# Performance work log

Hardware: AMD Instinct MI355X
Metric: run time of the kernel (lower is better)

## Reference

```python
import jax, jax.numpy as jnp
import numpy as np

B, C, N, K = 8, 192, 3136, 9
COUT = 384


def setup_inputs() -> dict:
    key = jax.random.key(0)
    k1, k2, k3, k4 = jax.random.split(key, 4)
    x = jax.random.normal(k1, (B, C, N, 1), dtype=jnp.float32)
    edge_index = jax.random.randint(k2, (2, B, N, K), 0, N, dtype=jnp.int64)
    # 1x1 conv params: BasicConv([2C, COUT]) with bias, act='relu'
    W = jax.random.normal(k3, (COUT, 2 * C), dtype=jnp.float32) * (1.0 / np.sqrt(2 * C))
    b = jax.random.normal(k4, (COUT,), dtype=jnp.float32) * 0.01
    return {"x": x, "edge_index": edge_index, "W": W, "b": b}


def _gather(xs, idx):
    # xs: [B, C, N]; idx: [B, N, K] -> [B, C, N, K]
    return jax.vmap(lambda xb, ib: xb[:, ib])(xs, idx)


def reference(x, edge_index, W, b):
    xs = x[..., 0]                       # [B, C, N]
    x_i = _gather(xs, edge_index[1])     # [B, C, N, K] center features
    x_j = _gather(xs, edge_index[0])     # [B, C, N, K] neighbor features
    feat = jnp.concatenate([x_i, x_j - x_i], axis=1)  # [B, 2C, N, K]
    # 1x1 conv + bias + relu
    h = jnp.einsum('oi,bink->bonk', W, feat) + b[None, :, None, None]
    h = jax.nn.relu(h)                   # [B, COUT, N, K]
    return jnp.max(h, axis=-1, keepdims=True)  # [B, COUT, N, 1]
```

## Files before the change

### kernel.cpp

```cpp
#include <hip/hip_runtime.h>
#include <hip/hip_bf16.h>


#define Bb   8
#define Cc   192
#define Nn   3136
#define Kk   9
#define CO   384
#define TWOC 384
#define JTOT 768
#define PADC 200

typedef short  short8 __attribute__((ext_vector_type(8)));
typedef float  f32x4  __attribute__((ext_vector_type(4)));

__device__ __forceinline__ float bf2f(unsigned int u16) {
    union { unsigned int i; float f; } c;
    c.i = u16 << 16;
    return c.f;
}
__device__ __forceinline__ float bflo(unsigned int u) {
    union { unsigned int i; float f; } c;
    c.i = u << 16;
    return c.f;
}
__device__ __forceinline__ float bfhi(unsigned int u) {
    union { unsigned int i; float f; } c;
    c.i = u & 0xffff0000u;
    return c.f;
}
__device__ __forceinline__ short f2bf(float f) {
    __hip_bfloat16 h = __float2bfloat16(f);
    short s; __builtin_memcpy(&s, &h, 2); return s;
}
__device__ __forceinline__ void gload16(const void* g, void* l) {
    __builtin_amdgcn_global_load_lds(
        (const __attribute__((address_space(1))) unsigned int*)g,
        (__attribute__((address_space(3))) unsigned int*)l, 16, 0, 0);
}

__global__ __launch_bounds__(256) void prep_fused(const void* __restrict__ x_,
                                                  const void* __restrict__ W_,
                                                  const int* __restrict__ ei,
                                                  short* __restrict__ xT,
                                                  short* __restrict__ A_Tb,
                                                  int* __restrict__ flags) {
    __shared__ float s[64][33];
    __shared__ int sflag;
    const int tid = threadIdx.x;
    const int bid = blockIdx.x;

    if (tid < 64) {
        unsigned int u = ((const unsigned short*)x_)[2 * tid];
        int bige = (((u >> 7) & 0xFFu) >= 0x88u);
        unsigned long long bf = __ballot(bige);
        int f32 = (bf != 0ull) ? 1 : 0;
        if (tid == 0) sflag = f32;
        if (bid == 0) {
            int oddnz = (ei[2 * tid + 1] != 0);
            unsigned long long bo = __ballot(oddnz);
            if (tid == 0) {
                flags[0] = f32;
                flags[1] = (bo == 0ull) ? 1 : 0;
            }
        }
    }
    __syncthreads();
    const int fp32 = sflag;

    if (bid < 2352) {
        int b   = bid / 294;
        int rem = bid - b * 294;
        int ct  = rem / 49;
        int nt  = rem - ct * 49;
        const int n0 = nt * 64;
        const int c0 = ct * 32;
        const int cl   = tid >> 3;
        const int nseg = tid & 7;

        if (fp32) {
            const float* p = (const float*)x_ + ((size_t)b * Cc + c0 + cl) * Nn + n0 + nseg * 8;
            float4 v0 = *(const float4*)p;
            float4 v1 = *(const float4*)(p + 4);
            int nb = nseg * 8;
            s[nb + 0][cl] = v0.x;  s[nb + 1][cl] = v0.y;
            s[nb + 2][cl] = v0.z;  s[nb + 3][cl] = v0.w;
            s[nb + 4][cl] = v1.x;  s[nb + 5][cl] = v1.y;
            s[nb + 6][cl] = v1.z;  s[nb + 7][cl] = v1.w;
        } else {
            const unsigned short* p = (const unsigned short*)x_ + ((size_t)b * Cc + c0 + cl) * Nn + n0 + nseg * 8;
            ushort4 u0 = *(const ushort4*)p;
            ushort4 u1 = *(const ushort4*)(p + 4);
            int nb = nseg * 8;
            s[nb + 0][cl] = bf2f(u0.x);  s[nb + 1][cl] = bf2f(u0.y);
            s[nb + 2][cl] = bf2f(u0.z);  s[nb + 3][cl] = bf2f(u0.w);
            s[nb + 4][cl] = bf2f(u1.x);  s[nb + 5][cl] = bf2f(u1.y);
            s[nb + 6][cl] = bf2f(u1.z);  s[nb + 7][cl] = bf2f(u1.w);
        }
        __syncthreads();

        const int nl = tid >> 2;
        const int cs = tid & 3;
        short8 o;
#pragma unroll
        for (int i = 0; i < 8; ++i) o[i] = f2bf(s[nl][cs * 8 + i]);
        *(short8*)(xT + ((size_t)b * Nn + n0 + nl) * PADC + c0 + cs * 8) = o;
    } else {
        int t = (bid - 2352) * 256 + tid;
        int j = t / Cc;
        int c = t - j * Cc;
        int row = (j < CO) ? j : (j - CO);
        float w1, w2;
        if (fp32) {
            const float* W = (const float*)W_;
            w1 = W[row * TWOC + c];  w2 = W[row * TWOC + Cc + c];
        } else {
            const unsigned short* W = (const unsigned short*)W_;
            w1 = bf2f(W[row * TWOC + c]);  w2 = bf2f(W[row * TWOC + Cc + c]);
        }
        A_Tb[(size_t)j * PADC + c] = f2bf((j < CO) ? (w1 - w2) : w2);
    }
}

__global__ __launch_bounds__(256, 3) void gemm_mfma(const short* __restrict__ xT,
                                                    const short* __restrict__ A_Tb,
                                                    short* __restrict__ T) {
    __shared__ short Asl[64 * PADC];
    __shared__ short Bsl[64 * PADC];

    const int n0 = blockIdx.x * 64;
    const int j0 = blockIdx.y * 64;
    const int b  = blockIdx.z;
    const int tid  = threadIdx.x;
    const int w    = tid >> 6;
    const int lane = tid & 63;
    const int col  = lane & 15;
    const int quad = lane >> 4;

    {
        const short* gA = xT   + ((size_t)b * Nn + n0) * PADC;
        const short* gB = A_Tb + (size_t)j0 * PADC;
#pragma unroll
        for (int c = w; c < 25; c += 4) {
            gload16(gA + c * 512 + lane * 8, Asl + c * 512);
            gload16(gB + c * 512 + lane * 8, Bsl + c * 512);
        }
    }
    __syncthreads();

    f32x4 acc[4];
#pragma unroll
    for (int i = 0; i < 4; ++i) acc[i] = (f32x4)(0.0f);

#pragma unroll
    for (int kf = 0; kf < 6; ++kf) {
        short8 bfr = *(const short8*)(Bsl + (w * 16 + col) * PADC + kf * 32 + quad * 8);
#pragma unroll
        for (int fm = 0; fm < 4; ++fm) {
            short8 a = *(const short8*)(Asl + (fm * 16 + col) * PADC + kf * 32 + quad * 8);
            acc[fm] = __builtin_amdgcn_mfma_f32_16x16x32_bf16(a, bfr, acc[fm], 0, 0, 0);
        }
    }
    __syncthreads();

    short* Ct = Asl;
#pragma unroll
    for (int fm = 0; fm < 4; ++fm) {
#pragma unroll
        for (int r = 0; r < 4; ++r) {
            Ct[(fm * 16 + quad * 4 + r) * 72 + w * 16 + col] = f2bf(acc[fm][r]);
        }
    }
    __syncthreads();

    {
        const int row = tid >> 2;
        const int gq  = tid & 3;
#pragma unroll
        for (int i = 0; i < 2; ++i) {
            int g = gq + i * 4;
            *(short8*)(T + ((size_t)(b * Nn + n0 + row)) * JTOT + j0 + g * 8) =
                *(const short8*)(Ct + row * 72 + g * 8);
        }
    }
}

__global__ __launch_bounds__(384) void gather_max(const int* __restrict__ ei,
                                                  const short* __restrict__ T,
                                                  const void* __restrict__ bias_,
                                                  void* __restrict__ out_,
                                                  const int* __restrict__ flags) {
    __shared__ float sm[32][97];
    __shared__ int soff0[32][Kk];
    __shared__ int soff1[32][Kk];

    const int fp32 = flags[0];
    const int is64 = flags[1];
    const int bid  = blockIdx.x;
    const int b    = bid & 7;
    const int rest = bid >> 3;
    const int quarter = rest / 98;
    const int n0   = (rest % 98) * 32;
    const int tid  = threadIdx.x;

    for (int s = tid; s < 32 * 2 * Kk; s += 384) {
        int ln = s / (2 * Kk);
        int slot = s - ln * (2 * Kk);
        int n = n0 + ln;
        size_t pos; int* dstp;
        if (slot < Kk) { pos = ((size_t)b * Nn + n) * Kk + slot;               dstp = &soff0[ln][slot]; }
        else           { pos = ((size_t)(Bb + b) * Nn + n) * Kk + (slot - Kk); dstp = &soff1[ln][slot - Kk]; }
        int v = is64 ? ei[2 * pos] : ei[pos];
        v = (v < 0) ? 0 : (v >= Nn ? Nn - 1 : v);
        *dstp = v * (JTOT * 2);
    }
    __syncthreads();

    const int cg  = tid % 12;
    const int seg = tid / 12;
    const int och = quarter * 96 + cg * 8;
    const char* Tb = (const char*)T + (size_t)b * Nn * JTOT * 2;
    const char* Tu = Tb + (size_t)och * 2;
    const char* Tv = Tb + (size_t)(CO + och) * 2;

    float bv[8];
    if (fp32) {
        const float* bp = (const float*)bias_ + och;
#pragma unroll
        for (int j = 0; j < 8; ++j) bv[j] = bp[j];
    } else {
        const unsigned short* bp = (const unsigned short*)bias_ + och;
#pragma unroll
        for (int j = 0; j < 8; ++j) bv[j] = bf2f(bp[j]);
    }

    float m0 = -INFINITY, m1 = -INFINITY, m2 = -INFINITY, m3 = -INFINITY;
    float m4 = -INFINITY, m5 = -INFINITY, m6 = -INFINITY, m7 = -INFINITY;
#pragma unroll
    for (int k = 0; k < Kk; ++k) {
        const int o1 = soff1[seg][k];
        const int o0 = soff0[seg][k];
        uint4 uu = *(const uint4*)(Tu + o1);
        uint4 vv = *(const uint4*)(Tv + o0);
        m0 = fmaxf(m0, bflo(uu.x) + bflo(vv.x));
        m1 = fmaxf(m1, bfhi(uu.x) + bfhi(vv.x));
        m2 = fmaxf(m2, bflo(uu.y) + bflo(vv.y));
        m3 = fmaxf(m3, bfhi(uu.y) + bfhi(vv.y));
        m4 = fmaxf(m4, bflo(uu.z) + bflo(vv.z));
        m5 = fmaxf(m5, bfhi(uu.z) + bfhi(vv.z));
        m6 = fmaxf(m6, bflo(uu.w) + bflo(vv.w));
        m7 = fmaxf(m7, bfhi(uu.w) + bfhi(vv.w));
    }
    sm[seg][cg * 8 + 0] = fmaxf(m0 + bv[0], 0.0f);
    sm[seg][cg * 8 + 1] = fmaxf(m1 + bv[1], 0.0f);
    sm[seg][cg * 8 + 2] = fmaxf(m2 + bv[2], 0.0f);
    sm[seg][cg * 8 + 3] = fmaxf(m3 + bv[3], 0.0f);
    sm[seg][cg * 8 + 4] = fmaxf(m4 + bv[4], 0.0f);
    sm[seg][cg * 8 + 5] = fmaxf(m5 + bv[5], 0.0f);
    sm[seg][cg * 8 + 6] = fmaxf(m6 + bv[6], 0.0f);
    sm[seg][cg * 8 + 7] = fmaxf(m7 + bv[7], 0.0f);
    __syncthreads();

    const int g = tid >> 5, l = tid & 31;
    if (fp32) {
        float* op = (float*)out_;
#pragma unroll
        for (int rr = 0; rr < 8; ++rr) {
            int ol = g * 8 + rr;
            int o  = quarter * 96 + ol;
            op[((size_t)b * CO + o) * Nn + n0 + l] = sm[l][ol];
        }
    } else {
        __hip_bfloat16* op = (__hip_bfloat16*)out_;
#pragma unroll
        for (int rr = 0; rr < 8; ++rr) {
            int ol = g * 8 + rr;
            int o  = quarter * 96 + ol;
            op[((size_t)b * CO + o) * Nn + n0 + l] = __float2bfloat16(sm[l][ol]);
        }
    }
}

extern "C" void kernel_launch(void* const* d_in, const int* in_sizes, int n_in,
                              void* d_out, int out_size, void* d_ws, size_t ws_size,
                              hipStream_t stream) {
    const void* x  = d_in[0];
    const int*  ei = (const int*)d_in[1];
    const void* W  = d_in[2];
    const void* bs = d_in[3];

    char* ws = (char*)d_ws;
    int*   flags = (int*)ws;
    short* A_Tb  = (short*)(ws + 1024);
    short* xT    = (short*)(ws + (512u << 10));
    short* T     = (short*)(ws + (11u << 20));

    prep_fused<<<2352 + 576, 256, 0, stream>>>(x, W, ei, xT, A_Tb, flags);

    dim3 g1(Nn / 64, JTOT / 64, Bb);
    gemm_mfma<<<g1, 256, 0, stream>>>(xT, A_Tb, T);

    gather_max<<<Bb * 4 * (Nn / 32), 384, 0, stream>>>(ei, T, bs, d_out, flags);
}
```

Measured before the change: 132.4 us.

## Fuse prep, GEMM and gather-max into one persistent cooperative kernel

```diff
diff --git a/kernel.cpp b/kernel.cpp
--- a/kernel.cpp
+++ b/kernel.cpp
@@ -1,5 +1,8 @@
 #include <hip/hip_runtime.h>
 #include <hip/hip_bf16.h>
+#include <hip/hip_cooperative_groups.h>
+
+namespace cg = cooperative_groups;
 
 
 #define Bb   8
@@ -39,244 +42,253 @@
         (__attribute__((address_space(3))) unsigned int*)l, 16, 0, 0);
 }
 
-__global__ __launch_bounds__(256) void prep_fused(const void* __restrict__ x_,
-                                                  const void* __restrict__ W_,
-                                                  const int* __restrict__ ei,
-                                                  short* __restrict__ xT,
-                                                  short* __restrict__ A_Tb,
-                                                  int* __restrict__ flags) {
-    __shared__ float s[64][33];
-    __shared__ int sflag;
+__global__ __launch_bounds__(256, 3) void fused_all(
+    const void* __restrict__ x_, const int* __restrict__ ei,
+    const void* __restrict__ W_, const void* __restrict__ bias_,
+    void* __restrict__ out_, short* __restrict__ xT,
+    short* __restrict__ A_Tb, short* __restrict__ T)
+{
+    cg::grid_group grid = cg::this_grid();
+    __shared__ char smem[51200];
+    __shared__ int sflag, sis64;
     const int tid = threadIdx.x;
     const int bid = blockIdx.x;
+    const int nblk = gridDim.x;
 
     if (tid < 64) {
         unsigned int u = ((const unsigned short*)x_)[2 * tid];
         int bige = (((u >> 7) & 0xFFu) >= 0x88u);
         unsigned long long bf = __ballot(bige);
-        int f32 = (bf != 0ull) ? 1 : 0;
-        if (tid == 0) sflag = f32;
-        if (bid == 0) {
-            int oddnz = (ei[2 * tid + 1] != 0);
-            unsigned long long bo = __ballot(oddnz);
-            if (tid == 0) {
-                flags[0] = f32;
-                flags[1] = (bo == 0ull) ? 1 : 0;
-            }
-        }
+        if (tid == 0) sflag = (bf != 0ull) ? 1 : 0;
+        int oddnz = (ei[2 * tid + 1] != 0);
+        unsigned long long bo = __ballot(oddnz);
+        if (tid == 0) sis64 = (bo == 0ull) ? 1 : 0;
     }
     __syncthreads();
     const int fp32 = sflag;
-
-    if (bid < 2352) {
-        int b   = bid / 294;
-        int rem = bid - b * 294;
-        int ct  = rem / 49;
-        int nt  = rem - ct * 49;
-        const int n0 = nt * 64;
-        const int c0 = ct * 32;
-        const int cl   = tid >> 3;
-        const int nseg = tid & 7;
-
-        if (fp32) {
-            const float* p = (const float*)x_ + ((size_t)b * Cc + c0 + cl) * Nn + n0 + nseg * 8;
-            float4 v0 = *(const float4*)p;
-            float4 v1 = *(const float4*)(p + 4);
-            int nb = nseg * 8;
-            s[nb + 0][cl] = v0.x;  s[nb + 1][cl] = v0.y;
-            s[nb + 2][cl] = v0.z;  s[nb + 3][cl] = v0.w;
-            s[nb + 4][cl] = v1.x;  s[nb + 5][cl] = v1.y;
-            s[nb + 6][cl] = v1.z;  s[nb + 7][cl] = v1.w;
-        } else {
-            const unsigned short* p = (const unsigned short*)x_ + ((size_t)b * Cc + c0 + cl) * Nn + n0 + nseg * 8;
-            ushort4 u0 = *(const ushort4*)p;
-            ushort4 u1 = *(const ushort4*)(p + 4);
-            int nb = nseg * 8;
-            s[nb + 0][cl] = bf2f(u0.x);  s[nb + 1][cl] = bf2f(u0.y);
-            s[nb + 2][cl] = bf2f(u0.z);  s[nb + 3][cl] = bf2f(u0.w);
-            s[nb + 4][cl] = bf2f(u1.x);  s[nb + 5][cl] = bf2f(u1.y);
-            s[nb + 6][cl] = bf2f(u1.z);  s[nb + 7][cl] = bf2f(u1.w);
+    const int is64 = sis64;
+
+    {
+        float (*s)[33] = (float (*)[33])smem;
+        for (int u = bid; u < 2928; u += nblk) {
+            if (u < 2352) {
+                int b   = u / 294;
+                int rem = u - b * 294;
+                int ct  = rem / 49;
+                int nt  = rem - ct * 49;
+                const int n0 = nt * 64;
+                const int c0 = ct * 32;
+                const int cl   = tid >> 3;
+                const int nseg = tid & 7;
+
+                if (fp32) {
+                    const float* p = (const float*)x_ + ((size_t)b * Cc + c0 + cl) * Nn + n0 + nseg * 8;
+                    float4 v0 = *(const float4*)p;
+                    float4 v1 = *(const float4*)(p + 4);
+                    int nb = nseg * 8;
+                    s[nb + 0][cl] = v0.x;  s[nb + 1][cl] = v0.y;
+                    s[nb + 2][cl] = v0.z;  s[nb + 3][cl] = v0.w;
+                    s[nb + 4][cl] = v1.x;  s[nb + 5][cl] = v1.y;
+                    s[nb + 6][cl] = v1.z;  s[nb + 7][cl] = v1.w;
+                } else {
+                    const unsigned short* p = (const unsigned short*)x_ + ((size_t)b * Cc + c0 + cl) * Nn + n0 + nseg * 8;
+                    ushort4 u0 = *(const ushort4*)p;
+                    ushort4 u1 = *(const ushort4*)(p + 4);
+                    int nb = nseg * 8;
+                    s[nb + 0][cl] = bf2f(u0.x);  s[nb + 1][cl] = bf2f(u0.y);
+                    s[nb + 2][cl] = bf2f(u0.z);  s[nb + 3][cl] = bf2f(u0.w);
+                    s[nb + 4][cl] = bf2f(u1.x);  s[nb + 5][cl] = bf2f(u1.y);
+                    s[nb + 6][cl] = bf2f(u1.z);  s[nb + 7][cl] = bf2f(u1.w);
+                }
+                __syncthreads();
+
+                const int nl = tid >> 2;
+                const int cs = tid & 3;
+                short8 o;
+#pragma unroll
+                for (int i = 0; i < 8; ++i) o[i] = f2bf(s[nl][cs * 8 + i]);
+                *(short8*)(xT + ((size_t)b * Nn + n0 + nl) * PADC + c0 + cs * 8) = o;
+            } else {
+                int t = (u - 2352) * 256 + tid;
+                int j = t / Cc;
+                int c = t - j * Cc;
+                int row = (j < CO) ? j : (j - CO);
+                float w1, w2;
+                if (fp32) {
+                    const float* W = (const float*)W_;
+                    w1 = W[row * TWOC + c];  w2 = W[row * TWOC + Cc + c];
+                } else {
+                    const unsigned short* W = (const unsigned short*)W_;
+                    w1 = bf2f(W[row * TWOC + c]);  w2 = bf2f(W[row * TWOC + Cc + c]);
+                }
+                A_Tb[(size_t)j * PADC + c] = f2bf((j < CO) ? (w1 - w2) : w2);
+            }
+            __syncthreads();
         }
-        __syncthreads();
-
-        const int nl = tid >> 2;
-        const int cs = tid & 3;
-        short8 o;
-#pragma unroll
-        for (int i = 0; i < 8; ++i) o[i] = f2bf(s[nl][cs * 8 + i]);
-        *(short8*)(xT + ((size_t)b * Nn + n0 + nl) * PADC + c0 + cs * 8) = o;
-    } else {
-        int t = (bid - 2352) * 256 + tid;
-        int j = t / Cc;
-        int c = t - j * Cc;
-        int row = (j < CO) ? j : (j - CO);
-        float w1, w2;
-        if (fp32) {
-            const float* W = (const float*)W_;
-            w1 = W[row * TWOC + c];  w2 = W[row * TWOC + Cc + c];
-        } else {
-            const unsigned short* W = (const unsigned short*)W_;
-            w1 = bf2f(W[row * TWOC + c]);  w2 = bf2f(W[row * TWOC + Cc + c]);
+    }
+    __threadfence();
+    grid.sync();
+
+    {
+        short* Asl = (short*)smem;
+        short* Bsl = (short*)(smem + 25600);
+        const int w    = tid >> 6;
+        const int lane = tid & 63;
+        const int col  = lane & 15;
+        const int quad = lane >> 4;
+
+        for (int t = bid; t < 4704; t += nblk) {
+            const int jt   = t % 12;
+            const int rest = t / 12;
+            const int b    = rest & 7;
+            const int nt   = rest >> 3;
+            const int n0 = nt * 64, j0 = jt * 64;
+
+            const short* gA = xT   + ((size_t)b * Nn + n0) * PADC;
+            const short* gB = A_Tb + (size_t)j0 * PADC;
+            for (int c = w; c < 25; c += 4) {
+                gload16(gA + c * 512 + lane * 8, Asl + c * 512);
+                gload16(gB + c * 512 + lane * 8, Bsl + c * 512);
+            }
+            __syncthreads();
+
+            f32x4 acc[4];
+#pragma unroll
+            for (int i = 0; i < 4; ++i) acc[i] = (f32x4)(0.0f);
+
+#pragma unroll
+            for (int kf = 0; kf < 6; ++kf) {
+                short8 bfr = *(const short8*)(Bsl + (w * 16 + col) * PADC + kf * 32 + quad * 8);
+#pragma unroll
+                for (int fm = 0; fm < 4; ++fm) {
+                    short8 a = *(const short8*)(Asl + (fm * 16 + col) * PADC + kf * 32 + quad * 8);
+                    acc[fm] = __builtin_amdgcn_mfma_f32_16x16x32_bf16(a, bfr, acc[fm], 0, 0, 0);
+                }
+            }
+            __syncthreads();
+
+            short* Ct = Asl;
+#pragma unroll
+            for (int fm = 0; fm < 4; ++fm) {
+#pragma unroll
+                for (int r = 0; r < 4; ++r) {
+                    Ct[(fm * 16 + quad * 4 + r) * 72 + w * 16 + col] = f2bf(acc[fm][r]);
+                }
+            }
+            __syncthreads();
+
+            {
+                const int row = tid >> 2;
+                const int gq  = tid & 3;
+#pragma unroll
+                for (int i = 0; i < 2; ++i) {
+                    int g = gq + i * 4;
+                    *(short8*)(T + ((size_t)(b * Nn + n0 + row)) * JTOT + j0 + g * 8) =
+                        *(const short8*)(Ct + row * 72 + g * 8);
+                }
+            }
+            __syncthreads();
         }
-        A_Tb[(size_t)j * PADC + c] = f2bf((j < CO) ? (w1 - w2) : w2);
-    }
-}
-
-__global__ __launch_bounds__(256, 3) void gemm_mfma(const short* __restrict__ xT,
-                                                    const short* __restrict__ A_Tb,
-                                                    short* __restrict__ T) {
-    __shared__ short Asl[64 * PADC];
-    __shared__ short Bsl[64 * PADC];
-
-    const int n0 = blockIdx.x * 64;
-    const int j0 = blockIdx.y * 64;
-    const int b  = blockIdx.z;
-    const int tid  = threadIdx.x;
-    const int w    = tid >> 6;
-    const int lane = tid & 63;
-    const int col  = lane & 15;
-    const int quad = lane >> 4;
+    }
+    __threadfence();
+    grid.sync();
 
     {
-        const short* gA = xT   + ((size_t)b * Nn + n0) * PADC;
-        const short* gB = A_Tb + (size_t)j0 * PADC;
-#pragma unroll
-        for (int c = w; c < 25; c += 4) {
-            gload16(gA + c * 512 + lane * 8, Asl + c * 512);
-            gload16(gB + c * 512 + lane * 8, Bsl + c * 512);
-        }
-    }
-    __syncthreads();
-
-    f32x4 acc[4];
-#pragma unroll
-    for (int i = 0; i < 4; ++i) acc[i] = (f32x4)(0.0f);
-
-#pragma unroll
-    for (int kf = 0; kf < 6; ++kf) {
-        short8 bfr = *(const short8*)(Bsl + (w * 16 + col) * PADC + kf * 32 + quad * 8);
-#pragma unroll
-        for (int fm = 0; fm < 4; ++fm) {
-            short8 a = *(const short8*)(Asl + (fm * 16 + col) * PADC + kf * 32 + quad * 8);
-            acc[fm] = __builtin_amdgcn_mfma_f32_16x16x32_bf16(a, bfr, acc[fm], 0, 0, 0);
-        }
-    }
-    __syncthreads();
-
-    short* Ct = Asl;
-#pragma unroll
-    for (int fm = 0; fm < 4; ++fm) {
-#pragma unroll
-        for (int r = 0; r < 4; ++r) {
-            Ct[(fm * 16 + quad * 4 + r) * 72 + w * 16 + col] = f2bf(acc[fm][r]);
-        }
-    }
-    __syncthreads();
-
-    {
-        const int row = tid >> 2;
-        const int gq  = tid & 3;
-#pragma unroll
-        for (int i = 0; i < 2; ++i) {
-            int g = gq + i * 4;
-            *(short8*)(T + ((size_t)(b * Nn + n0 + row)) * JTOT + j0 + g * 8) =
-                *(const short8*)(Ct + row * 72 + g * 8);
-        }
-    }
-}
-
-__global__ __launch_bounds__(384) void gather_max(const int* __restrict__ ei,
-                                                  const short* __restrict__ T,
-                                                  const void* __restrict__ bias_,
-                                                  void* __restrict__ out_,
-                                                  const int* __restrict__ flags) {
-    __shared__ float sm[32][97];
-    __shared__ int soff0[32][Kk];
-    __shared__ int soff1[32][Kk];
-
-    const int fp32 = flags[0];
-    const int is64 = flags[1];
-    const int bid  = blockIdx.x;
-    const int b    = bid & 7;
-    const int rest = bid >> 3;
-    const int quarter = rest / 98;
-    const int n0   = (rest % 98) * 32;
-    const int tid  = threadIdx.x;
-
-    for (int s = tid; s < 32 * 2 * Kk; s += 384) {
-        int ln = s / (2 * Kk);
-        int slot = s - ln * (2 * Kk);
-        int n = n0 + ln;
-        size_t pos; int* dstp;
-        if (slot < Kk) { pos = ((size_t)b * Nn + n) * Kk + slot;               dstp = &soff0[ln][slot]; }
-        else           { pos = ((size_t)(Bb + b) * Nn + n) * Kk + (slot - Kk); dstp = &soff1[ln][slot - Kk]; }
-        int v = is64 ? ei[2 * pos] : ei[pos];
-        v = (v < 0) ? 0 : (v >= Nn ? Nn - 1 : v);
-        *dstp = v * (JTOT * 2);
-    }
-    __syncthreads();
-
-    const int cg  = tid % 12;
-    const int seg = tid / 12;
-    const int och = quarter * 96 + cg * 8;
-    const char* Tb = (const char*)T + (size_t)b * Nn * JTOT * 2;
-    const char* Tu = Tb + (size_t)och * 2;
-    const char* Tv = Tb + (size_t)(CO + och) * 2;
-
-    float bv[8];
-    if (fp32) {
-        const float* bp = (const float*)bias_ + och;
-#pragma unroll
-        for (int j = 0; j < 8; ++j) bv[j] = bp[j];
-    } else {
-        const unsigned short* bp = (const unsigned short*)bias_ + och;
-#pragma unroll
-        for (int j = 0; j < 8; ++j) bv[j] = bf2f(bp[j]);
-    }
-
-    float m0 = -INFINITY, m1 = -INFINITY, m2 = -INFINITY, m3 = -INFINITY;
-    float m4 = -INFINITY, m5 = -INFINITY, m6 = -INFINITY, m7 = -INFINITY;
-#pragma unroll
-    for (int k = 0; k < Kk; ++k) {
-        const int o1 = soff1[seg][k];
-        const int o0 = soff0[seg][k];
-        uint4 uu = *(const uint4*)(Tu + o1);
-        uint4 vv = *(const uint4*)(Tv + o0);
-        m0 = fmaxf(m0, bflo(uu.x) + bflo(vv.x));
-        m1 = fmaxf(m1, bfhi(uu.x) + bfhi(vv.x));
-        m2 = fmaxf(m2, bflo(uu.y) + bflo(vv.y));
-        m3 = fmaxf(m3, bfhi(uu.y) + bfhi(vv.y));
-        m4 = fmaxf(m4, bflo(uu.z) + bflo(vv.z));
-        m5 = fmaxf(m5, bfhi(uu.z) + bfhi(vv.z));
-        m6 = fmaxf(m6, bflo(uu.w) + bflo(vv.w));
-        m7 = fmaxf(m7, bfhi(uu.w) + bfhi(vv.w));
-    }
-    sm[seg][cg * 8 + 0] = fmaxf(m0 + bv[0], 0.0f);
-    sm[seg][cg * 8 + 1] = fmaxf(m1 + bv[1], 0.0f);
-    sm[seg][cg * 8 + 2] = fmaxf(m2 + bv[2], 0.0f);
-    sm[seg][cg * 8 + 3] = fmaxf(m3 + bv[3], 0.0f);
-    sm[seg][cg * 8 + 4] = fmaxf(m4 + bv[4], 0.0f);
-    sm[seg][cg * 8 + 5] = fmaxf(m5 + bv[5], 0.0f);
-    sm[seg][cg * 8 + 6] = fmaxf(m6 + bv[6], 0.0f);
-    sm[seg][cg * 8 + 7] = fmaxf(m7 + bv[7], 0.0f);
-    __syncthreads();
-
-    const int g = tid >> 5, l = tid & 31;
-    if (fp32) {
-        float* op = (float*)out_;
-#pragma unroll
-        for (int rr = 0; rr < 8; ++rr) {
-            int ol = g * 8 + rr;
-            int o  = quarter * 96 + ol;
-            op[((size_t)b * CO + o) * Nn + n0 + l] = sm[l][ol];
-        }
-    } else {
-        __hip_bfloat16* op = (__hip_bfloat16*)out_;
-#pragma unroll
-        for (int rr = 0; rr < 8; ++rr) {
-            int ol = g * 8 + rr;
-            int o  = quarter * 96 + ol;
-            op[((size_t)b * CO + o) * Nn + n0 + l] = __float2bfloat16(sm[l][ol]);
+        float (*sm)[129]  = (float (*)[129])smem;
+        int (*soff0)[Kk]  = (int (*)[Kk])(smem + 16512);
+        int (*soff1)[Kk]  = (int (*)[Kk])(smem + 17664);
+        const int b   = bid & 7;
+        const int pb  = nblk >> 3;
+        const char* Tb = (const char*)T + (size_t)b * Nn * JTOT * 2;
+        const int cgi = tid & 7;
+        const int seg = tid >> 3;
+
+        for (int s = (bid >> 3); s < 294; s += pb) {
+            const int third = s / 98;
+            const int nt    = s - third * 98;
+            const int n0    = nt * 32;
+
+            for (int q = tid; q < 32 * 2 * Kk; q += 256) {
+                int ln = q / (2 * Kk);
+                int slot = q - ln * (2 * Kk);
+                int n = n0 + ln;
+                size_t pos; int* dstp;
+                if (slot < Kk) { pos = ((size_t)b * Nn + n) * Kk + slot;               dstp = &soff0[ln][slot]; }
+                else           { pos = ((size_t)(Bb + b) * Nn + n) * Kk + (slot - Kk); dstp = &soff1[ln][slot - Kk]; }
+                int v = is64 ? ei[2 * pos] : ei[pos];
+                v = (v < 0) ? 0 : (v >= Nn ? Nn - 1 : v);
+                *dstp = v * (JTOT * 2);
+            }
+            __syncthreads();
+
+            const int och = third * 128 + cgi * 16;
+            const char* Tu = Tb + (size_t)och * 2;
+            const char* Tv = Tb + (size_t)(CO + och) * 2;
+
+            float bv[16];
+            if (fp32) {
+                const float* bp = (const float*)bias_ + och;
+#pragma unroll
+                for (int j = 0; j < 16; ++j) bv[j] = bp[j];
+            } else {
+                const unsigned short* bp = (const unsigned short*)bias_ + och;
+#pragma unroll
+                for (int j = 0; j < 16; ++j) bv[j] = bf2f(bp[j]);
+            }
+
+            float mm[16];
+#pragma unroll
+            for (int j = 0; j < 16; ++j) mm[j] = -INFINITY;
+
+#pragma unroll
+            for (int k = 0; k < Kk; ++k) {
+                const int o1 = soff1[seg][k];
+                const int o0 = soff0[seg][k];
+                uint4 ua = *(const uint4*)(Tu + o1);
+                uint4 ub = *(const uint4*)(Tu + o1 + 16);
+                uint4 va = *(const uint4*)(Tv + o0);
+                uint4 vb = *(const uint4*)(Tv + o0 + 16);
+                mm[0]  = fmaxf(mm[0],  bflo(ua.x) + bflo(va.x));
+                mm[1]  = fmaxf(mm[1],  bfhi(ua.x) + bfhi(va.x));
+                mm[2]  = fmaxf(mm[2],  bflo(ua.y) + bflo(va.y));
+                mm[3]  = fmaxf(mm[3],  bfhi(ua.y) + bfhi(va.y));
+                mm[4]  = fmaxf(mm[4],  bflo(ua.z) + bflo(va.z));
+                mm[5]  = fmaxf(mm[5],  bfhi(ua.z) + bfhi(va.z));
+                mm[6]  = fmaxf(mm[6],  bflo(ua.w) + bflo(va.w));
+                mm[7]  = fmaxf(mm[7],  bfhi(ua.w) + bfhi(va.w));
+                mm[8]  = fmaxf(mm[8],  bflo(ub.x) + bflo(vb.x));
+                mm[9]  = fmaxf(mm[9],  bfhi(ub.x) + bfhi(vb.x));
+                mm[10] = fmaxf(mm[10], bflo(ub.y) + bflo(vb.y));
+                mm[11] = fmaxf(mm[11], bfhi(ub.y) + bfhi(vb.y));
+                mm[12] = fmaxf(mm[12], bflo(ub.z) + bflo(vb.z));
+                mm[13] = fmaxf(mm[13], bfhi(ub.z) + bfhi(vb.z));
+                mm[14] = fmaxf(mm[14], bflo(ub.w) + bflo(vb.w));
+                mm[15] = fmaxf(mm[15], bfhi(ub.w) + bfhi(vb.w));
+            }
+#pragma unroll
+            for (int j = 0; j < 16; ++j)
+                sm[seg][cgi * 16 + j] = fmaxf(mm[j] + bv[j], 0.0f);
+            __syncthreads();
+
+            const int g = tid >> 5, l = tid & 31;
+            if (fp32) {
+                float* op = (float*)out_;
+#pragma unroll
+                for (int rr = 0; rr < 16; ++rr) {
+                    int ol = g * 16 + rr;
+                    int o  = third * 128 + ol;
+                    op[((size_t)b * CO + o) * Nn + n0 + l] = sm[l][ol];
+                }
+            } else {
+                __hip_bfloat16* op = (__hip_bfloat16*)out_;
+#pragma unroll
+                for (int rr = 0; rr < 16; ++rr) {
+                    int ol = g * 16 + rr;
+                    int o  = third * 128 + ol;
+                    op[((size_t)b * CO + o) * Nn + n0 + l] = __float2bfloat16(sm[l][ol]);
+                }
+            }
+            __syncthreads();
         }
     }
 }
@@ -288,17 +300,25 @@
     const int*  ei = (const int*)d_in[1];
     const void* W  = d_in[2];
     const void* bs = d_in[3];
+    void* out = d_out;
 
     char* ws = (char*)d_ws;
-    int*   flags = (int*)ws;
     short* A_Tb  = (short*)(ws + 1024);
     short* xT    = (short*)(ws + (512u << 10));
     short* T     = (short*)(ws + (11u << 20));
 
-    prep_fused<<<2352 + 576, 256, 0, stream>>>(x, W, ei, xT, A_Tb, flags);
-
-    dim3 g1(Nn / 64, JTOT / 64, Bb);
-    gemm_mfma<<<g1, 256, 0, stream>>>(xT, A_Tb, T);
-
-    gather_max<<<Bb * 4 * (Nn / 32), 384, 0, stream>>>(ei, T, bs, d_out, flags);
-}
+    static int nblk = 0;
+    if (nblk == 0) {
+        int maxb = 0;
+        hipOccupancyMaxActiveBlocksPerMultiprocessor(&maxb, fused_all, 256, 0);
+        if (maxb < 1) maxb = 1;
+        if (maxb > 3) maxb = 3;
+        nblk = (maxb * 256) & ~7;
+        if (nblk < 8) nblk = 8;
+    }
+
+    void* args[] = {(void*)&x, (void*)&ei, (void*)&W, (void*)&bs,
+                    (void*)&out, (void*)&xT, (void*)&A_Tb, (void*)&T};
+    hipLaunchCooperativeKernel((void*)fused_all, dim3(nblk), dim3(256),
+                               args, 0, stream);
+}
```

New measurement: 277.6 us. +109.6%, slower.
